# Kernel tuning notes

Hardware: AMD Instinct MI355X
Metric: run time of the kernel (lower is better)

Reference implementation:

```python
import jax, jax.numpy as jnp
import numpy as np
from jax import lax

WIN = 7                      # skimage default win_size
NP_ = WIN * WIN              # pixels per window (2D)
COV_NORM = NP_ / (NP_ - 1)   # sample covariance normalization (use_sample_covariance=True)
K1, K2 = 0.01, 0.03          # skimage defaults


def setup_inputs() -> dict:
    key = jax.random.key(0)
    k1, k2 = jax.random.split(key)
    B, H, W = 64, 512, 512
    predictions = jax.random.uniform(k1, (B, H, W), dtype=jnp.float32)
    labels = jax.random.uniform(k2, (B, H, W), dtype=jnp.float32)
    return {"predictions": predictions, "labels": labels}


def _mean_filter(x):
    # x: [B, 1, H, W] -> valid 7x7 mean filter. Because skimage crops `pad`
    # border pixels before averaging, a VALID convolution reproduces exactly
    # the pixels that survive the crop (reflect padding never enters them).
    kern = jnp.full((1, 1, WIN, WIN), 1.0 / NP_, dtype=x.dtype)
    return lax.conv_general_dilated(x, kern, (1, 1), 'VALID')


def reference(predictions, labels):
    X = predictions[:, None].astype(jnp.float32)  # [B,1,H,W]
    Y = labels[:, None].astype(jnp.float32)

    # per-sample data_range = max(pred,targ) - min(pred,targ)
    dmax = jnp.maximum(X.max(axis=(1, 2, 3)), Y.max(axis=(1, 2, 3)))
    dmin = jnp.minimum(X.min(axis=(1, 2, 3)), Y.min(axis=(1, 2, 3)))
    dr = (dmax - dmin)[:, None, None, None]       # [B,1,1,1]
    C1 = (K1 * dr) ** 2
    C2 = (K2 * dr) ** 2

    ux = _mean_filter(X)
    uy = _mean_filter(Y)
    uxx = _mean_filter(X * X)
    uyy = _mean_filter(Y * Y)
    uxy = _mean_filter(X * Y)

    vx = COV_NORM * (uxx - ux * ux)
    vy = COV_NORM * (uyy - uy * uy)
    vxy = COV_NORM * (uxy - ux * uy)

    S = ((2.0 * ux * uy + C1) * (2.0 * vxy + C2)) / (
        (ux * ux + uy * uy + C1) * (vx + vy + C2))

    mssim = S.mean(axis=(1, 2, 3))  # per-sample SSIM
    return mssim.mean()             # ssim_total / batch_size
```

## Files before the change

kernel.cpp:

```cpp
#include <hip/hip_runtime.h>

#define Hc     512
#define Wc     512
#define OH     506
#define OW     506
#define NPIX   (Hc * Wc)
#define BATCH  64
#define CHUNKS 16

#define BH     16
#define NBAND  32
#define NW     3
#define WPB    4
#define BLK_PER_STRIP (NBAND / WPB)
#define NSTRIP (BATCH * NW)
#define NBLK   (NSTRIP * BLK_PER_STRIP)
#define STRIPS_PER_XCD (NSTRIP / 8)
#define NPART  NBLK

typedef float f32x2 __attribute__((ext_vector_type(2)));
typedef float f32x4 __attribute__((ext_vector_type(4)));

__global__ __launch_bounds__(256) void mm_part_kernel(
    const float* __restrict__ X, const float* __restrict__ Y,
    float* __restrict__ part)
{
    int blk = blockIdx.x;
    int b   = blk >> 4;
    int ch  = blk & 15;
    size_t base = (size_t)b * NPIX + (size_t)ch * (NPIX / CHUNKS);
    const float4* x4 = (const float4*)(X + base);
    const float4* y4 = (const float4*)(Y + base);
    const int n4 = (NPIX / CHUNKS) / 4;

    float mn = 1e38f, mx = -1e38f;
    for (int i = threadIdx.x; i < n4; i += 256) {
        float4 a = x4[i];
        float4 c = y4[i];
        mn = fminf(mn, fminf(fminf(a.x, a.y), fminf(a.z, a.w)));
        mx = fmaxf(mx, fmaxf(fmaxf(a.x, a.y), fmaxf(a.z, a.w)));
        mn = fminf(mn, fminf(fminf(c.x, c.y), fminf(c.z, c.w)));
        mx = fmaxf(mx, fmaxf(fmaxf(c.x, c.y), fmaxf(c.z, c.w)));
    }
    #pragma unroll
    for (int off = 1; off < 64; off <<= 1) {
        mn = fminf(mn, __shfl_xor(mn, off, 64));
        mx = fmaxf(mx, __shfl_xor(mx, off, 64));
    }
    __shared__ float smn[4], smx[4];
    int lane = threadIdx.x & 63, wid = threadIdx.x >> 6;
    if (lane == 0) { smn[wid] = mn; smx[wid] = mx; }
    __syncthreads();
    if (threadIdx.x == 0) {
        mn = fminf(fminf(smn[0], smn[1]), fminf(smn[2], smn[3]));
        mx = fmaxf(fmaxf(smx[0], smx[1]), fmaxf(smx[2], smx[3]));
        part[2 * blk]     = mn;
        part[2 * blk + 1] = mx;
    }
}

__global__ __launch_bounds__(256, 8) void ssim_stream_kernel(
    const float* __restrict__ X, const float* __restrict__ Y,
    const float* __restrict__ mmpart, float* __restrict__ part)
{
    const int lane = threadIdx.x & 63;
    const int wid  = threadIdx.x >> 6;

    const int lin   = blockIdx.x;
    const int xcd   = lin & 7;
    const int slot  = lin >> 3;
    const int strip_local = slot >> 3;
    const int blk   = slot & 7;
    const int strip = xcd * STRIPS_PER_XCD + strip_local;
    const int img   = strip / NW;
    const int chunk = strip - img * NW;
    const int band  = blk * WPB + wid;

    float mn = 1e38f, mx = -1e38f;
    #pragma unroll
    for (int ch = 0; ch < CHUNKS; ++ch) {
        mn = fminf(mn, mmpart[2 * (img * CHUNKS + ch)]);
        mx = fmaxf(mx, mmpart[2 * (img * CHUNKS + ch) + 1]);
    }
    const float dr = mx - mn;
    const float C1 = (0.01f * dr) * (0.01f * dr);
    const float C2 = (0.03f * dr) * (0.03f * dr);
    const f32x2 C1v = {C1, C1};
    const f32x2 C2v = {C2, C2};
    const f32x2 inv2  = {1.0f / 49.0f, 1.0f / 49.0f};
    const f32x2 covn2 = {49.0f / 48.0f, 49.0f / 48.0f};

    const int cbase  = (chunk == 0) ? 0 : (chunk == 1) ? 248 : 496;
    const int out_lo = (chunk == 0) ? 0 : (chunk == 1) ? 250 : 498;
    const int out_hi = (chunk == 0) ? 249 : (chunk == 1) ? 497 : 505;

    const int col0  = cbase + 4 * lane;
    const int col0c = (col0 < 508) ? col0 : 508;
    f32x2 vm01, vm23;
    {
        float v[4];
        #pragma unroll
        for (int j = 0; j < 4; ++j) {
            int oc = col0 + j;
            v[j] = (oc >= out_lo && oc <= out_hi) ? 1.0f : 0.0f;
        }
        vm01 = (f32x2){v[0], v[1]};
        vm23 = (f32x2){v[2], v[3]};
    }

    const int oy0 = band * BH;
    const int nvalid = (OH - oy0) < BH ? (OH - oy0) : BH;

    const float* px = X + (size_t)img * NPIX + col0c;
    const float* py = Y + (size_t)img * NPIX + col0c;

    f32x2 Vx[2]  = {{0,0},{0,0}}, Vy[2]  = {{0,0},{0,0}};
    f32x2 Vxy[2] = {{0,0},{0,0}}, Vss[2] = {{0,0},{0,0}};

    #define VADD(xa, ya)                                                     \
    {                                                                        \
        f32x2 xl = (xa).lo, xh = (xa).hi, yl = (ya).lo, yh = (ya).hi;        \
        Vx[0] += xl; Vx[1] += xh; Vy[0] += yl; Vy[1] += yh;                  \
        Vxy[0] += xl * yl; Vxy[1] += xh * yh;                                \
        Vss[0] += xl * xl + yl * yl; Vss[1] += xh * xh + yh * yh;            \
    }
    #define VSUB(xa, ya)                                                     \
    {                                                                        \
        f32x2 xl = (xa).lo, xh = (xa).hi, yl = (ya).lo, yh = (ya).hi;        \
        Vx[0] -= xl; Vx[1] -= xh; Vy[0] -= yl; Vy[1] -= yh;                  \
        Vxy[0] -= xl * yl; Vxy[1] -= xh * yh;                                \
        Vss[0] -= xl * xl + yl * yl; Vss[1] -= xh * xh + yh * yh;            \
    }

    #pragma unroll
    for (int k = 0; k < 6; ++k) {
        f32x4 xa = *(const f32x4*)(px + (size_t)(oy0 + k) * Wc);
        f32x4 ya = *(const f32x4*)(py + (size_t)(oy0 + k) * Wc);
        VADD(xa, ya)
    }

    f32x2 acc2 = {0.f, 0.f};

    #define H7(V, W0, W1, W2, W3)                                            \
    {                                                                        \
        float v0 = V[0].x, v1 = V[0].y, v2 = V[1].x, v3 = V[1].y;            \
        float t01 = v0 + v1, u23 = v2 + v3;                                  \
        float P3 = t01 + v2, P4 = t01 + u23;                                 \
        float A3 = __shfl_down(P3, 1, 64);                                   \
        float A4 = __shfl_down(P4, 1, 64);                                   \
        float B1 = __shfl_down(v0, 2, 64);                                   \
        float B2 = __shfl_down(t01, 2, 64);                                  \
        float cc = u23 + A4;                                                 \
        W0 = P4 + A3;                                                        \
        W1 = cc + v1;                                                        \
        W2 = cc + B1;                                                        \
        W3 = (v3 + A4) + B2;                                                 \
    }

    #define SSIM2(wx, wy, wp, ws, vmv)                                       \
    {                                                                        \
        f32x2 ux   = wx * inv2;                                              \
        f32x2 uy   = wy * inv2;                                              \
        f32x2 uxuy = ux * uy;                                                \
        f32x2 u2   = ux * ux + uy * uy;                                      \
        f32x2 vxy  = (wp * inv2 - uxuy) * covn2;                             \
        f32x2 vss  = (ws * inv2 - u2) * covn2;                               \
        f32x2 A1   = uxuy + uxuy + C1v;                                      \
        f32x2 A2   = vxy + vxy + C2v;                                        \
        f32x2 B1   = u2 + C1v;                                               \
        f32x2 B2   = vss + C2v;                                              \
        f32x2 den  = B1 * B2;                                                \
        f32x2 num  = A1 * A2;                                                \
        f32x2 rv   = {__builtin_amdgcn_rcpf(den.x),                          \
                      __builtin_amdgcn_rcpf(den.y)};                         \
        acc2 += num * rv * vmv;                                              \
    }

    const float* pxi = px + (size_t)(oy0 + 6) * Wc;
    const float* pyi = py + (size_t)(oy0 + 6) * Wc;
    const float* pxo = px + (size_t)oy0 * Wc;
    const float* pyo = py + (size_t)oy0 * Wc;

    #pragma unroll 2
    for (int tt = 0; tt < nvalid; ++tt) {
        f32x4 xi = *(const f32x4*)pxi; pxi += Wc;
        f32x4 yi = *(const f32x4*)pyi; pyi += Wc;
        VADD(xi, yi)
        float Wx0, Wx1, Wx2, Wx3;  H7(Vx,  Wx0, Wx1, Wx2, Wx3)
        float Wy0, Wy1, Wy2, Wy3;  H7(Vy,  Wy0, Wy1, Wy2, Wy3)
        float Wp0, Wp1, Wp2, Wp3;  H7(Vxy, Wp0, Wp1, Wp2, Wp3)
        float Ws0, Ws1, Ws2, Ws3;  H7(Vss, Ws0, Ws1, Ws2, Ws3)
        f32x2 wx01 = {Wx0, Wx1}, wx23 = {Wx2, Wx3};
        f32x2 wy01 = {Wy0, Wy1}, wy23 = {Wy2, Wy3};
        f32x2 wp01 = {Wp0, Wp1}, wp23 = {Wp2, Wp3};
        f32x2 ws01 = {Ws0, Ws1}, ws23 = {Ws2, Ws3};
        SSIM2(wx01, wy01, wp01, ws01, vm01)
        SSIM2(wx23, wy23, wp23, ws23, vm23)
        f32x4 xo = *(const f32x4*)pxo; pxo += Wc;
        f32x4 yo = *(const f32x4*)pyo; pyo += Wc;
        VSUB(xo, yo)
    }

    #undef SSIM2
    #undef H7
    #undef VADD
    #undef VSUB

    float acc = acc2.x + acc2.y;
    #pragma unroll
    for (int off = 1; off < 64; off <<= 1)
        acc += __shfl_xor(acc, off, 64);
    __shared__ float sacc[4];
    if (lane == 0) sacc[wid] = acc;
    __syncthreads();
    if (threadIdx.x == 0)
        part[lin] = (sacc[0] + sacc[1]) + (sacc[2] + sacc[3]);
}

__global__ __launch_bounds__(1024) void final_reduce_kernel(
    const float* __restrict__ part, float* __restrict__ out)
{
    __shared__ double sd[1024];
    double s = 0.0;
    for (int i = threadIdx.x; i < NPART; i += 1024)
        s += (double)part[i];
    sd[threadIdx.x] = s;
    __syncthreads();
    for (int off = 512; off > 0; off >>= 1) {
        if (threadIdx.x < off) sd[threadIdx.x] += sd[threadIdx.x + off];
        __syncthreads();
    }
    if (threadIdx.x == 0)
        out[0] = (float)(sd[0] / ((double)BATCH * OH * OW));
}

extern "C" void kernel_launch(void* const* d_in, const int* in_sizes, int n_in,
                              void* d_out, int out_size, void* d_ws, size_t ws_size,
                              hipStream_t stream) {
    const float* X = (const float*)d_in[0];
    const float* Y = (const float*)d_in[1];
    float* out = (float*)d_out;
    float* ws  = (float*)d_ws;

    float* mmpart = ws;
    float* part   = ws + 2048;

    mm_part_kernel<<<BATCH * CHUNKS, 256, 0, stream>>>(X, Y, mmpart);
    ssim_stream_kernel<<<NBLK, 64 * WPB, 0, stream>>>(X, Y, mmpart, part);
    final_reduce_kernel<<<1, 1024, 0, stream>>>(part, out);
}
```

Before: 75.35 us.

## Process full image width per wave with 8 columns per lane and halved band height

Each lane now covers 8 contiguous columns, so one 64-lane wave spans a whole 512-wide row. This removes the three overlapping column chunks and their duplicated halo loads and masking. The horizontal 7-tap sum is rebuilt from prefix sums plus neighbour shuffles, and band height drops from 16 to 8 rows to keep the block count up. The cost is more registers per thread, with the launch-bounds occupancy hint lowered from 8 to 4, and the vertical 6-row warm-up is now amortized over fewer output rows.

```diff
diff --git a/kernel.cpp b/kernel.cpp
--- a/kernel.cpp
+++ b/kernel.cpp
@@ -8,14 +8,12 @@
 #define BATCH  64
 #define CHUNKS 16
 
-#define BH     16
-#define NBAND  32
-#define NW     3
+#define BH     8
+#define NBAND  64
 #define WPB    4
-#define BLK_PER_STRIP (NBAND / WPB)
-#define NSTRIP (BATCH * NW)
-#define NBLK   (NSTRIP * BLK_PER_STRIP)
-#define STRIPS_PER_XCD (NSTRIP / 8)
+#define BLK_PER_IMG (NBAND / WPB)
+#define NBLK   (BATCH * BLK_PER_IMG)
+#define IMGS_PER_XCD (BATCH / 8)
 #define NPART  NBLK
 
 typedef float f32x2 __attribute__((ext_vector_type(2)));
@@ -59,22 +57,19 @@
     }
 }
 
-__global__ __launch_bounds__(256, 8) void ssim_stream_kernel(
+__global__ __launch_bounds__(256, 4) void ssim_stream_kernel(
     const float* __restrict__ X, const float* __restrict__ Y,
     const float* __restrict__ mmpart, float* __restrict__ part)
 {
     const int lane = threadIdx.x & 63;
     const int wid  = threadIdx.x >> 6;
 
-    const int lin   = blockIdx.x;
-    const int xcd   = lin & 7;
-    const int slot  = lin >> 3;
-    const int strip_local = slot >> 3;
-    const int blk   = slot & 7;
-    const int strip = xcd * STRIPS_PER_XCD + strip_local;
-    const int img   = strip / NW;
-    const int chunk = strip - img * NW;
-    const int band  = blk * WPB + wid;
+    const int lin  = blockIdx.x;
+    const int xcd  = lin & 7;
+    const int slot = lin >> 3;
+    const int img  = xcd * IMGS_PER_XCD + (slot >> 4);
+    const int blk  = slot & 15;
+    const int band = blk * WPB + wid;
 
     float mn = 1e38f, mx = -1e38f;
     #pragma unroll
@@ -90,71 +85,77 @@
     const f32x2 inv2  = {1.0f / 49.0f, 1.0f / 49.0f};
     const f32x2 covn2 = {49.0f / 48.0f, 49.0f / 48.0f};
 
-    const int cbase  = (chunk == 0) ? 0 : (chunk == 1) ? 248 : 496;
-    const int out_lo = (chunk == 0) ? 0 : (chunk == 1) ? 250 : 498;
-    const int out_hi = (chunk == 0) ? 249 : (chunk == 1) ? 497 : 505;
-
-    const int col0  = cbase + 4 * lane;
-    const int col0c = (col0 < 508) ? col0 : 508;
-    f32x2 vm01, vm23;
-    {
-        float v[4];
-        #pragma unroll
-        for (int j = 0; j < 4; ++j) {
-            int oc = col0 + j;
-            v[j] = (oc >= out_lo && oc <= out_hi) ? 1.0f : 0.0f;
-        }
-        vm01 = (f32x2){v[0], v[1]};
-        vm23 = (f32x2){v[2], v[3]};
+    f32x2 vm01 = {1.f, 1.f}, vm23 = {1.f, 1.f};
+    f32x2 vm45 = {1.f, 1.f}, vm67 = {1.f, 1.f};
+    if (lane == 63) {
+        vm23 = (f32x2){0.f, 0.f};
+        vm45 = (f32x2){0.f, 0.f};
+        vm67 = (f32x2){0.f, 0.f};
     }
 
     const int oy0 = band * BH;
     const int nvalid = (OH - oy0) < BH ? (OH - oy0) : BH;
 
-    const float* px = X + (size_t)img * NPIX + col0c;
-    const float* py = Y + (size_t)img * NPIX + col0c;
-
-    f32x2 Vx[2]  = {{0,0},{0,0}}, Vy[2]  = {{0,0},{0,0}};
-    f32x2 Vxy[2] = {{0,0},{0,0}}, Vss[2] = {{0,0},{0,0}};
-
-    #define VADD(xa, ya)                                                     \
-    {                                                                        \
-        f32x2 xl = (xa).lo, xh = (xa).hi, yl = (ya).lo, yh = (ya).hi;        \
-        Vx[0] += xl; Vx[1] += xh; Vy[0] += yl; Vy[1] += yh;                  \
-        Vxy[0] += xl * yl; Vxy[1] += xh * yh;                                \
-        Vss[0] += xl * xl + yl * yl; Vss[1] += xh * xh + yh * yh;            \
-    }
-    #define VSUB(xa, ya)                                                     \
-    {                                                                        \
-        f32x2 xl = (xa).lo, xh = (xa).hi, yl = (ya).lo, yh = (ya).hi;        \
-        Vx[0] -= xl; Vx[1] -= xh; Vy[0] -= yl; Vy[1] -= yh;                  \
-        Vxy[0] -= xl * yl; Vxy[1] -= xh * yh;                                \
-        Vss[0] -= xl * xl + yl * yl; Vss[1] -= xh * xh + yh * yh;            \
+    const float* px = X + (size_t)img * NPIX + 8 * lane;
+    const float* py = Y + (size_t)img * NPIX + 8 * lane;
+
+    f32x2 Vx[4]  = {{0,0},{0,0},{0,0},{0,0}};
+    f32x2 Vy[4]  = {{0,0},{0,0},{0,0},{0,0}};
+    f32x2 Vxy[4] = {{0,0},{0,0},{0,0},{0,0}};
+    f32x2 Vss[4] = {{0,0},{0,0},{0,0},{0,0}};
+
+    #define VADD8(xa0, xa1, ya0, ya1)                                        \
+    {                                                                        \
+        f32x2 x0 = (xa0).lo, x1 = (xa0).hi, x2 = (xa1).lo, x3 = (xa1).hi;    \
+        f32x2 y0 = (ya0).lo, y1 = (ya0).hi, y2 = (ya1).lo, y3 = (ya1).hi;    \
+        Vx[0] += x0; Vx[1] += x1; Vx[2] += x2; Vx[3] += x3;                  \
+        Vy[0] += y0; Vy[1] += y1; Vy[2] += y2; Vy[3] += y3;                  \
+        Vxy[0] += x0 * y0; Vxy[1] += x1 * y1;                                \
+        Vxy[2] += x2 * y2; Vxy[3] += x3 * y3;                                \
+        Vss[0] += x0 * x0 + y0 * y0; Vss[1] += x1 * x1 + y1 * y1;            \
+        Vss[2] += x2 * x2 + y2 * y2; Vss[3] += x3 * x3 + y3 * y3;            \
+    }
+    #define VSUB8(xa0, xa1, ya0, ya1)                                        \
+    {                                                                        \
+        f32x2 x0 = (xa0).lo, x1 = (xa0).hi, x2 = (xa1).lo, x3 = (xa1).hi;    \
+        f32x2 y0 = (ya0).lo, y1 = (ya0).hi, y2 = (ya1).lo, y3 = (ya1).hi;    \
+        Vx[0] -= x0; Vx[1] -= x1; Vx[2] -= x2; Vx[3] -= x3;                  \
+        Vy[0] -= y0; Vy[1] -= y1; Vy[2] -= y2; Vy[3] -= y3;                  \
+        Vxy[0] -= x0 * y0; Vxy[1] -= x1 * y1;                                \
+        Vxy[2] -= x2 * y2; Vxy[3] -= x3 * y3;                                \
+        Vss[0] -= x0 * x0 + y0 * y0; Vss[1] -= x1 * x1 + y1 * y1;            \
+        Vss[2] -= x2 * x2 + y2 * y2; Vss[3] -= x3 * x3 + y3 * y3;            \
     }
 
     #pragma unroll
     for (int k = 0; k < 6; ++k) {
-        f32x4 xa = *(const f32x4*)(px + (size_t)(oy0 + k) * Wc);
-        f32x4 ya = *(const f32x4*)(py + (size_t)(oy0 + k) * Wc);
-        VADD(xa, ya)
+        const float* rx = px + (size_t)(oy0 + k) * Wc;
+        const float* ry = py + (size_t)(oy0 + k) * Wc;
+        f32x4 xa0 = *(const f32x4*)rx;
+        f32x4 xa1 = *(const f32x4*)(rx + 4);
+        f32x4 ya0 = *(const f32x4*)ry;
+        f32x4 ya1 = *(const f32x4*)(ry + 4);
+        VADD8(xa0, xa1, ya0, ya1)
     }
 
     f32x2 acc2 = {0.f, 0.f};
 
-    #define H7(V, W0, W1, W2, W3)                                            \
-    {                                                                        \
-        float v0 = V[0].x, v1 = V[0].y, v2 = V[1].x, v3 = V[1].y;            \
-        float t01 = v0 + v1, u23 = v2 + v3;                                  \
-        float P3 = t01 + v2, P4 = t01 + u23;                                 \
-        float A3 = __shfl_down(P3, 1, 64);                                   \
-        float A4 = __shfl_down(P4, 1, 64);                                   \
-        float B1 = __shfl_down(v0, 2, 64);                                   \
-        float B2 = __shfl_down(t01, 2, 64);                                  \
-        float cc = u23 + A4;                                                 \
-        W0 = P4 + A3;                                                        \
-        W1 = cc + v1;                                                        \
-        W2 = cc + B1;                                                        \
-        W3 = (v3 + A4) + B2;                                                 \
+    #define H7_8(V, Wa, Wb, Wc_, Wd)                                         \
+    {                                                                        \
+        float c0 = V[0].x, c1 = V[0].y, c2 = V[1].x, c3 = V[1].y;            \
+        float c4 = V[2].x, c5 = V[2].y, c6 = V[3].x, c7 = V[3].y;            \
+        float P1 = c0,      P2 = P1 + c1, P3 = P2 + c2, P4 = P3 + c3;        \
+        float P5 = P4 + c4, P6 = P5 + c5, P7 = P6 + c6, P8 = P7 + c7;        \
+        float N1 = __shfl_down(P1, 1, 64);                                   \
+        float N2 = __shfl_down(P2, 1, 64);                                   \
+        float N3 = __shfl_down(P3, 1, 64);                                   \
+        float N4 = __shfl_down(P4, 1, 64);                                   \
+        float N5 = __shfl_down(P5, 1, 64);                                   \
+        float N6 = __shfl_down(P6, 1, 64);                                   \
+        Wa = (f32x2){P7,             P8 - P1};                               \
+        Wb = (f32x2){(P8 + N1) - P2, (P8 + N2) - P3};                        \
+        Wc_ = (f32x2){(P8 + N3) - P4, (P8 + N4) - P5};                       \
+        Wd = (f32x2){(P8 + N5) - P6, (P8 + N6) - P7};                        \
     }
 
     #define SSIM2(wx, wy, wp, ws, vmv)                                       \
@@ -183,28 +184,33 @@
 
     #pragma unroll 2
     for (int tt = 0; tt < nvalid; ++tt) {
-        f32x4 xi = *(const f32x4*)pxi; pxi += Wc;
-        f32x4 yi = *(const f32x4*)pyi; pyi += Wc;
-        VADD(xi, yi)
-        float Wx0, Wx1, Wx2, Wx3;  H7(Vx,  Wx0, Wx1, Wx2, Wx3)
-        float Wy0, Wy1, Wy2, Wy3;  H7(Vy,  Wy0, Wy1, Wy2, Wy3)
-        float Wp0, Wp1, Wp2, Wp3;  H7(Vxy, Wp0, Wp1, Wp2, Wp3)
-        float Ws0, Ws1, Ws2, Ws3;  H7(Vss, Ws0, Ws1, Ws2, Ws3)
-        f32x2 wx01 = {Wx0, Wx1}, wx23 = {Wx2, Wx3};
-        f32x2 wy01 = {Wy0, Wy1}, wy23 = {Wy2, Wy3};
-        f32x2 wp01 = {Wp0, Wp1}, wp23 = {Wp2, Wp3};
-        f32x2 ws01 = {Ws0, Ws1}, ws23 = {Ws2, Ws3};
-        SSIM2(wx01, wy01, wp01, ws01, vm01)
-        SSIM2(wx23, wy23, wp23, ws23, vm23)
-        f32x4 xo = *(const f32x4*)pxo; pxo += Wc;
-        f32x4 yo = *(const f32x4*)pyo; pyo += Wc;
-        VSUB(xo, yo)
+        f32x4 xi0 = *(const f32x4*)pxi;
+        f32x4 xi1 = *(const f32x4*)(pxi + 4); pxi += Wc;
+        f32x4 yi0 = *(const f32x4*)pyi;
+        f32x4 yi1 = *(const f32x4*)(pyi + 4); pyi += Wc;
+        VADD8(xi0, xi1, yi0, yi1)
+
+        f32x2 Wx01, Wx23, Wx45, Wx67;  H7_8(Vx,  Wx01, Wx23, Wx45, Wx67)
+        f32x2 Wy01, Wy23, Wy45, Wy67;  H7_8(Vy,  Wy01, Wy23, Wy45, Wy67)
+        f32x2 Wp01, Wp23, Wp45, Wp67;  H7_8(Vxy, Wp01, Wp23, Wp45, Wp67)
+        f32x2 Ws01, Ws23, Ws45, Ws67;  H7_8(Vss, Ws01, Ws23, Ws45, Ws67)
+
+        SSIM2(Wx01, Wy01, Wp01, Ws01, vm01)
+        SSIM2(Wx23, Wy23, Wp23, Ws23, vm23)
+        SSIM2(Wx45, Wy45, Wp45, Ws45, vm45)
+        SSIM2(Wx67, Wy67, Wp67, Ws67, vm67)
+
+        f32x4 xo0 = *(const f32x4*)pxo;
+        f32x4 xo1 = *(const f32x4*)(pxo + 4); pxo += Wc;
+        f32x4 yo0 = *(const f32x4*)pyo;
+        f32x4 yo1 = *(const f32x4*)(pyo + 4); pyo += Wc;
+        VSUB8(xo0, xo1, yo0, yo1)
     }
 
     #undef SSIM2
-    #undef H7
-    #undef VADD
-    #undef VSUB
+    #undef H7_8
+    #undef VADD8
+    #undef VSUB8
 
     float acc = acc2.x + acc2.y;
     #pragma unroll
```

Measured after the change: 91.99 us. +22.1%, slower.
